# Optimization experiments

Measured on AMD Instinct MI355X. Metric: run time of the kernel, lower is better.

Reference implementation:

```python
import jax, jax.numpy as jnp
import numpy as np


def setup_inputs() -> dict:
    key = jax.random.key(0)
    k0, k1, k2, k3 = jax.random.split(key, 4)
    B, C, D, H, W = 2, 64, 48, 96, 96
    KS = 3
    x = jax.random.normal(k0, (B, C, D, H, W), jnp.float32)
    # Conv3d 1x1 kernels collapse to dense [out, in] matrices
    qkv_w = jax.random.normal(k1, (3 * C, C), jnp.float32) * (1.0 / np.sqrt(C))
    qkv_b = jnp.zeros((3 * C,), jnp.float32)
    out_w = jax.random.normal(k2, (C, C), jnp.float32) * (1.0 / np.sqrt(C))
    out_b = jnp.zeros((C,), jnp.float32)
    rel_pos = jax.random.normal(k3, (C, KS, KS, KS), jnp.float32)
    return {"x": x, "qkv_w": qkv_w, "qkv_b": qkv_b,
            "out_w": out_w, "out_b": out_b, "rel_pos": rel_pos}


def reference(x, qkv_w, qkv_b, out_w, out_b, rel_pos):
    B, C, D, H, W = x.shape
    ks = rel_pos.shape[1]
    p = ks // 2
    # 1x1x1 conv == per-voxel dense projection
    qkv = jnp.einsum('bcdhw,oc->bodhw', x, qkv_w) + qkv_b[None, :, None, None, None]
    Q, K, V = jnp.split(qkv, 3, axis=1)
    pad = ((0, 0), (0, 0), (p, p), (p, p), (p, p))
    Kp = jnp.pad(K, pad)
    Vp = jnp.pad(V, pad)
    scale = 1.0 / np.sqrt(C)
    # attention logits over the ks^3 shifted windows (static slices, fixed small loop)
    logits = []
    for i in range(ks):
        for j in range(ks):
            for k in range(ks):
                Ks = Kp[:, :, i:i + D, j:j + H, k:k + W] \
                    + rel_pos[:, i, j, k][None, :, None, None, None]
                logits.append(jnp.sum(Q * Ks, axis=1) * scale)  # [B,D,H,W]
    attn = jax.nn.softmax(jnp.stack(logits, axis=1), axis=1)  # [B,ks^3,D,H,W]
    # weighted sum of shifted V windows, accumulated onto residual x (forward_v1)
    out = x
    idx = 0
    for i in range(ks):
        for j in range(ks):
            for k in range(ks):
                out = out + attn[:, idx][:, None] * Vp[:, :, i:i + D, j:j + H, k:k + W]
                idx += 1
    return jnp.einsum('bcdhw,oc->bodhw', out, out_w) + out_b[None, :, None, None, None]
```

## Files before the change

kernel.cpp:

```cpp
#include <hip/hip_runtime.h>
#include <hip/hip_bf16.h>

#define Sd 442368
#define HWc 9216
#define Wc 96
#define Hc 96
#define Dc 48

typedef unsigned short u16;
typedef unsigned int u32;
typedef __attribute__((ext_vector_type(8))) short short8;
typedef __attribute__((ext_vector_type(4))) float f32x4;

static __device__ __forceinline__ u16 f2bf(float f){
    __hip_bfloat16 h = __float2bfloat16(f);
    return *reinterpret_cast<u16*>(&h);
}
static __device__ __forceinline__ u32 pk2(float a, float b){
    return ((u32)f2bf(b) << 16) | (u32)f2bf(a);
}
static __device__ __forceinline__ float bflo(u32 u){ return __uint_as_float(u << 16); }
static __device__ __forceinline__ float bfhi(u32 u){ return __uint_as_float(u & 0xffff0000u); }

static __device__ __forceinline__ short8 ldfrag_w(const float* p){
    float4 f0 = *reinterpret_cast<const float4*>(p);
    float4 f1 = *reinterpret_cast<const float4*>(p + 4);
    union { short8 s; u32 u[4]; } r;
    r.u[0] = pk2(f0.x, f0.y); r.u[1] = pk2(f0.z, f0.w);
    r.u[2] = pk2(f1.x, f1.y); r.u[3] = pk2(f1.z, f1.w);
    return r.s;
}

#define NBLK_A 3456
__global__ __launch_bounds__(256, 2) void kv_mfma(
    const float* __restrict__ x, const float* __restrict__ qkv_w,
    const float* __restrict__ qkv_b, u16* __restrict__ KV)
{
    int bid = blockIdx.x;
    bid = (bid & 7) * (NBLK_A / 8) + (bid >> 3);
    int batch = bid / (NBLK_A / 2);
    int s0 = (bid - batch * (NBLK_A / 2)) * 256;
    int t = threadIdx.x, lane = t & 63, wv = t >> 6;
    int lo = lane & 15, hi = lane >> 4;
    __shared__ u16 L[256 * 72];

    const float* xb = x + (size_t)batch * 64 * Sd + s0;
    {
        u32 pk[32];
#pragma unroll
        for (int c = 0; c < 64; c += 2){
            float f0 = xb[(size_t)c * Sd + t];
            float f1 = xb[(size_t)(c + 1) * Sd + t];
            pk[c >> 1] = pk2(f0, f1);
        }
#pragma unroll
        for (int k = 0; k < 8; ++k){
            uint4 u; u.x = pk[k*4+0]; u.y = pk[k*4+1]; u.z = pk[k*4+2]; u.w = pk[k*4+3];
            *reinterpret_cast<uint4*>(&L[t * 72 + k * 8]) = u;
        }
    }
    __syncthreads();

    short8 af[8][2];
    f32x4  bias[8];
#pragma unroll
    for (int mt = 0; mt < 8; ++mt){
#pragma unroll
        for (int kh = 0; kh < 2; ++kh)
            af[mt][kh] = ldfrag_w(qkv_w + (size_t)(64 + mt*16 + lo) * 64 + kh*32 + hi*8);
        bias[mt] = *reinterpret_cast<const f32x4*>(qkv_b + 64 + mt*16 + hi*4);
    }

#pragma unroll
    for (int nt = 0; nt < 4; ++nt){
        int vl = wv * 64 + nt * 16 + lo;
        const u16* br = &L[vl * 72 + hi * 8];
        short8 b0 = *reinterpret_cast<const short8*>(br);
        short8 b1 = *reinterpret_cast<const short8*>(br + 32);
        u16* kvrow = KV + (size_t)(batch * Sd + s0 + vl) * 128 + hi * 4;
#pragma unroll
        for (int mt = 0; mt < 8; ++mt){
            f32x4 acc = bias[mt];
            acc = __builtin_amdgcn_mfma_f32_16x16x32_bf16(af[mt][0], b0, acc, 0, 0, 0);
            acc = __builtin_amdgcn_mfma_f32_16x16x32_bf16(af[mt][1], b1, acc, 0, 0, 0);
            uint2 st; st.x = pk2(acc[0], acc[1]); st.y = pk2(acc[2], acc[3]);
            *reinterpret_cast<uint2*>(kvrow + mt * 16) = st;
        }
    }
}

#define NBLK_B 6912
__global__ __launch_bounds__(256, 4) void attn_mfma2(
    const float* __restrict__ x, const float* __restrict__ qkv_w,
    const float* __restrict__ qkv_b, const float* __restrict__ out_w,
    const float* __restrict__ out_b, const float* __restrict__ rel_pos,
    const u16* __restrict__ KV, float* __restrict__ out)
{
    int bid = blockIdx.x;
    bid = (bid & 7) * (NBLK_B / 8) + (bid >> 3);
    int batch = bid / (NBLK_B / 2);
    int s0 = (bid - batch * (NBLK_B / 2)) * 128;
    int t = threadIdx.x, lane = t & 63, wv = t >> 6;
    int lo = lane & 15, hi = lane >> 4;
    int vt = t >> 1, half = t & 1;

    __shared__ u16 Lx[128 * 72];
    __shared__ u16 Lq[128 * 72];
    float* Lr = reinterpret_cast<float*>(Lx);

    const float* xb = x + (size_t)batch * 64 * Sd + s0;
    {
        u32 pk[16];
#pragma unroll
        for (int c2 = 0; c2 < 32; c2 += 2){
            float f0 = xb[(size_t)(half*32 + c2) * Sd + vt];
            float f1 = xb[(size_t)(half*32 + c2 + 1) * Sd + vt];
            pk[c2 >> 1] = pk2(f0, f1);
        }
#pragma unroll
        for (int k = 0; k < 4; ++k){
            uint4 u; u.x = pk[k*4+0]; u.y = pk[k*4+1]; u.z = pk[k*4+2]; u.w = pk[k*4+3];
            *reinterpret_cast<uint4*>(&Lx[vt * 72 + half * 32 + k * 8]) = u;
        }
    }
    __syncthreads();

    {
        short8 qa[4][2];
        f32x4  qbias[4];
#pragma unroll
        for (int mt = 0; mt < 4; ++mt){
#pragma unroll
            for (int kh = 0; kh < 2; ++kh)
                qa[mt][kh] = ldfrag_w(qkv_w + (size_t)(mt*16 + lo) * 64 + kh*32 + hi*8);
            qbias[mt] = *reinterpret_cast<const f32x4*>(qkv_b + mt*16 + hi*4);
        }
#pragma unroll
        for (int nt = 0; nt < 2; ++nt){
            int vl = wv * 32 + nt * 16 + lo;
            const u16* br = &Lx[vl * 72 + hi * 8];
            short8 b0 = *reinterpret_cast<const short8*>(br);
            short8 b1 = *reinterpret_cast<const short8*>(br + 32);
#pragma unroll
            for (int mt = 0; mt < 4; ++mt){
                f32x4 acc = qbias[mt];
                acc = __builtin_amdgcn_mfma_f32_16x16x32_bf16(qa[mt][0], b0, acc, 0, 0, 0);
                acc = __builtin_amdgcn_mfma_f32_16x16x32_bf16(qa[mt][1], b1, acc, 0, 0, 0);
                uint2 st; st.x = pk2(acc[0], acc[1]); st.y = pk2(acc[2], acc[3]);
                *reinterpret_cast<uint2*>(&Lq[vl * 72 + mt * 16 + hi * 4]) = st;
            }
        }
    }
    __syncthreads();

    float acc[32], Q[32];
    {
        const u16* xr = &Lx[vt * 72 + half * 32];
        const u16* qr = &Lq[vt * 72 + half * 32];
#pragma unroll
        for (int k = 0; k < 4; ++k){
            uint4 xa = *reinterpret_cast<const uint4*>(xr + k * 8);
            uint4 qa = *reinterpret_cast<const uint4*>(qr + k * 8);
            acc[k*8+0] = bflo(xa.x); acc[k*8+1] = bfhi(xa.x);
            acc[k*8+2] = bflo(xa.y); acc[k*8+3] = bfhi(xa.y);
            acc[k*8+4] = bflo(xa.z); acc[k*8+5] = bfhi(xa.z);
            acc[k*8+6] = bflo(xa.w); acc[k*8+7] = bfhi(xa.w);
            Q[k*8+0] = bflo(qa.x); Q[k*8+1] = bfhi(qa.x);
            Q[k*8+2] = bflo(qa.y); Q[k*8+3] = bfhi(qa.y);
            Q[k*8+4] = bflo(qa.z); Q[k*8+5] = bfhi(qa.z);
            Q[k*8+6] = bflo(qa.w); Q[k*8+7] = bfhi(qa.w);
        }
    }
    __syncthreads();

    {
        short8 ra[2][2];
#pragma unroll
        for (int mt = 0; mt < 2; ++mt){
            int o = mt * 16 + lo;
#pragma unroll
            for (int kh = 0; kh < 2; ++kh){
                float f[8];
#pragma unroll
                for (int j = 0; j < 8; ++j){
                    int k = kh * 32 + hi * 8 + j;
                    f[j] = (o < 27) ? rel_pos[k * 27 + o] : 0.f;
                }
                union { short8 s; u32 u[4]; } r;
                r.u[0] = pk2(f[0], f[1]); r.u[1] = pk2(f[2], f[3]);
                r.u[2] = pk2(f[4], f[5]); r.u[3] = pk2(f[6], f[7]);
                ra[mt][kh] = r.s;
            }
        }
#pragma unroll
        for (int nt = 0; nt < 2; ++nt){
            int vl = wv * 32 + nt * 16 + lo;
            const u16* br = &Lq[vl * 72 + hi * 8];
            short8 b0 = *reinterpret_cast<const short8*>(br);
            short8 b1 = *reinterpret_cast<const short8*>(br + 32);
            f32x4 a0 = {0.f, 0.f, 0.f, 0.f};
            f32x4 a1 = {0.f, 0.f, 0.f, 0.f};
            a0 = __builtin_amdgcn_mfma_f32_16x16x32_bf16(ra[0][0], b0, a0, 0, 0, 0);
            a0 = __builtin_amdgcn_mfma_f32_16x16x32_bf16(ra[0][1], b1, a0, 0, 0, 0);
            a1 = __builtin_amdgcn_mfma_f32_16x16x32_bf16(ra[1][0], b0, a1, 0, 0, 0);
            a1 = __builtin_amdgcn_mfma_f32_16x16x32_bf16(ra[1][1], b1, a1, 0, 0, 0);
#pragma unroll
            for (int j = 0; j < 4; ++j)
                Lr[vl * 29 + hi * 4 + j] = a0[j];
#pragma unroll
            for (int j = 0; j < 4; ++j){
                int row = 16 + hi * 4 + j;
                if (row < 27) Lr[vl * 29 + row] = a1[j];
            }
        }
    }
    __syncthreads();

    int s = s0 + vt;
    int d = s / HWc; int r = s - d * HWc; int h = r / Wc; int w = r - h * Wc;
    const u16* kvb = KV + ((size_t)batch * Sd + s) * 128 + half * 32;

    float lg[27];
#pragma unroll
    for (int o = 0; o < 27; ++o){
        const int di = o / 9 - 1, dj = (o / 3) % 3 - 1, dk = o % 3 - 1;
        bool inb = ((unsigned)(d + di) < (unsigned)Dc) &&
                   ((unsigned)(h + dj) < (unsigned)Hc) &&
                   ((unsigned)(w + dk) < (unsigned)Wc);
        float dsum = 0.f;
        if (inb){
            const u16* kp = kvb + (ptrdiff_t)(di * HWc + dj * Wc + dk) * 128;
            float d0 = 0.f, d1 = 0.f, d2 = 0.f, d3 = 0.f;
#pragma unroll
            for (int k = 0; k < 4; ++k){
                uint4 kk = *reinterpret_cast<const uint4*>(kp + k * 8);
                d0 += bflo(kk.x) * Q[k*8+0]; d1 += bfhi(kk.x) * Q[k*8+1];
                d2 += bflo(kk.y) * Q[k*8+2]; d3 += bfhi(kk.y) * Q[k*8+3];
                d0 += bflo(kk.z) * Q[k*8+4]; d1 += bfhi(kk.z) * Q[k*8+5];
                d2 += bflo(kk.w) * Q[k*8+6]; d3 += bfhi(kk.w) * Q[k*8+7];
            }
            dsum = (d0 + d1) + (d2 + d3);
        }
        lg[o] = dsum;
    }
#pragma unroll
    for (int o = 0; o < 27; ++o){
        float other = __shfl_xor(lg[o], 1);
        lg[o] = 0.125f * (lg[o] + other + Lr[vt * 29 + o]);
    }

    float m = lg[0];
#pragma unroll
    for (int o = 1; o < 27; ++o) m = fmaxf(m, lg[o]);
    float ssum = 0.f;
#pragma unroll
    for (int o = 0; o < 27; ++o){ lg[o] = __expf(lg[o] - m); ssum += lg[o]; }
    float inv = 1.f / ssum;

#pragma unroll
    for (int o = 0; o < 27; ++o){
        const int di = o / 9 - 1, dj = (o / 3) % 3 - 1, dk = o % 3 - 1;
        bool inb = ((unsigned)(d + di) < (unsigned)Dc) &&
                   ((unsigned)(h + dj) < (unsigned)Hc) &&
                   ((unsigned)(w + dk) < (unsigned)Wc);
        if (!inb) continue;
        float a = lg[o] * inv;
        const u16* vp = kvb + (ptrdiff_t)(di * HWc + dj * Wc + dk) * 128 + 64;
#pragma unroll
        for (int k = 0; k < 4; ++k){
            uint4 vv = *reinterpret_cast<const uint4*>(vp + k * 8);
            acc[k*8+0] += a * bflo(vv.x); acc[k*8+1] += a * bfhi(vv.x);
            acc[k*8+2] += a * bflo(vv.y); acc[k*8+3] += a * bfhi(vv.y);
            acc[k*8+4] += a * bflo(vv.z); acc[k*8+5] += a * bfhi(vv.z);
            acc[k*8+6] += a * bflo(vv.w); acc[k*8+7] += a * bfhi(vv.w);
        }
    }

#pragma unroll
    for (int k = 0; k < 4; ++k){
        uint4 u;
        u.x = pk2(acc[k*8+0], acc[k*8+1]); u.y = pk2(acc[k*8+2], acc[k*8+3]);
        u.z = pk2(acc[k*8+4], acc[k*8+5]); u.w = pk2(acc[k*8+6], acc[k*8+7]);
        *reinterpret_cast<uint4*>(&Lq[vt * 72 + half * 32 + k * 8]) = u;
    }
    __syncthreads();

    {
        short8 oa[4][2];
        f32x4  obias[4];
#pragma unroll
        for (int mt = 0; mt < 4; ++mt){
#pragma unroll
            for (int kh = 0; kh < 2; ++kh)
                oa[mt][kh] = ldfrag_w(out_w + (size_t)(mt*16 + lo) * 64 + kh*32 + hi*8);
            obias[mt] = *reinterpret_cast<const f32x4*>(out_b + mt*16 + hi*4);
        }
#pragma unroll
        for (int nt = 0; nt < 2; ++nt){
            int vl = wv * 32 + nt * 16 + lo;
            const u16* br = &Lq[vl * 72 + hi * 8];
            short8 b0 = *reinterpret_cast<const short8*>(br);
            short8 b1 = *reinterpret_cast<const short8*>(br + 32);
#pragma unroll
            for (int mt = 0; mt < 4; ++mt){
                f32x4 a4 = obias[mt];
                a4 = __builtin_amdgcn_mfma_f32_16x16x32_bf16(oa[mt][0], b0, a4, 0, 0, 0);
                a4 = __builtin_amdgcn_mfma_f32_16x16x32_bf16(oa[mt][1], b1, a4, 0, 0, 0);
                float* op = out + ((size_t)batch * 64 + mt*16 + hi*4) * Sd + (s0 + vl);
                op[0]              = a4[0];
                op[(size_t)Sd]     = a4[1];
                op[(size_t)2*Sd]   = a4[2];
                op[(size_t)3*Sd]   = a4[3];
            }
        }
    }
}

extern "C" void kernel_launch(void* const* d_in, const int* in_sizes, int n_in,
                              void* d_out, int out_size, void* d_ws, size_t ws_size,
                              hipStream_t stream) {
    const float* x       = (const float*)d_in[0];
    const float* qkv_w   = (const float*)d_in[1];
    const float* qkv_b   = (const float*)d_in[2];
    const float* out_w   = (const float*)d_in[3];
    const float* out_b   = (const float*)d_in[4];
    const float* rel_pos = (const float*)d_in[5];
    float* out = (float*)d_out;
    u16* KV = (u16*)d_ws;

    kv_mfma<<<NBLK_A, 256, 0, stream>>>(x, qkv_w, qkv_b, KV);
    attn_mfma2<<<NBLK_B, 256, 0, stream>>>(x, qkv_w, qkv_b, out_w, out_b,
                                           rel_pos, KV, out);
}
```

Baseline: 690.0 us.

## Fuse logits, softmax and V accumulation into a single online-softmax pass

Replaces the two-pass neighbourhood loop (logits, then softmax, then weighted V) with one pass that loads K and V together per neighbour and keeps a lazily rescaled running max and sum. Neighbour addresses are clamped without branches, the math uses packed float2 operations, and the scale is folded into exp2. Block barriers are dropped where each wave only reads the shared-memory rows it wrote itself, and the residual is now read from global fp32. This cuts repeated K/V traffic and barrier stalls, but the lazy rescale adds wave-wide votes and extra registers.

Result: slower. 766.3 us (+11.1%).

```diff
diff --git a/kernel.cpp b/kernel.cpp
--- a/kernel.cpp
+++ b/kernel.cpp
@@ -11,6 +11,7 @@
 typedef unsigned int u32;
 typedef __attribute__((ext_vector_type(8))) short short8;
 typedef __attribute__((ext_vector_type(4))) float f32x4;
+typedef __attribute__((ext_vector_type(2))) float f32x2;
 
 static __device__ __forceinline__ u16 f2bf(float f){
     __hip_bfloat16 h = __float2bfloat16(f);
@@ -21,6 +22,9 @@
 }
 static __device__ __forceinline__ float bflo(u32 u){ return __uint_as_float(u << 16); }
 static __device__ __forceinline__ float bfhi(u32 u){ return __uint_as_float(u & 0xffff0000u); }
+static __device__ __forceinline__ f32x2 unp2(u32 u){
+    f32x2 r; r.x = __uint_as_float(u << 16); r.y = __uint_as_float(u & 0xffff0000u); return r;
+}
 
 static __device__ __forceinline__ short8 ldfrag_w(const float* p){
     float4 f0 = *reinterpret_cast<const float4*>(p);
@@ -59,7 +63,6 @@
             *reinterpret_cast<uint4*>(&L[t * 72 + k * 8]) = u;
         }
     }
-    __syncthreads();
 
     short8 af[8][2];
     f32x4  bias[8];
@@ -90,7 +93,9 @@
 }
 
 #define NBLK_B 6912
-__global__ __launch_bounds__(256, 4) void attn_mfma2(
+#define SCLOG 0.18033688011112042f
+
+__global__ __launch_bounds__(256, 4) void attn_fused(
     const float* __restrict__ x, const float* __restrict__ qkv_w,
     const float* __restrict__ qkv_b, const float* __restrict__ out_w,
     const float* __restrict__ out_b, const float* __restrict__ rel_pos,
@@ -104,9 +109,8 @@
     int lo = lane & 15, hi = lane >> 4;
     int vt = t >> 1, half = t & 1;
 
-    __shared__ u16 Lx[128 * 72];
-    __shared__ u16 Lq[128 * 72];
-    float* Lr = reinterpret_cast<float*>(Lx);
+    __shared__ u16  Lx[128 * 72];
+    __shared__ float Lr[128 * 27];
 
     const float* xb = x + (size_t)batch * 64 * Sd + s0;
     {
@@ -123,7 +127,6 @@
             *reinterpret_cast<uint4*>(&Lx[vt * 72 + half * 32 + k * 8]) = u;
         }
     }
-    __syncthreads();
 
     {
         short8 qa[4][2];
@@ -147,31 +150,10 @@
                 acc = __builtin_amdgcn_mfma_f32_16x16x32_bf16(qa[mt][0], b0, acc, 0, 0, 0);
                 acc = __builtin_amdgcn_mfma_f32_16x16x32_bf16(qa[mt][1], b1, acc, 0, 0, 0);
                 uint2 st; st.x = pk2(acc[0], acc[1]); st.y = pk2(acc[2], acc[3]);
-                *reinterpret_cast<uint2*>(&Lq[vl * 72 + mt * 16 + hi * 4]) = st;
+                *reinterpret_cast<uint2*>(&Lx[vl * 72 + mt * 16 + hi * 4]) = st;
             }
         }
     }
-    __syncthreads();
-
-    float acc[32], Q[32];
-    {
-        const u16* xr = &Lx[vt * 72 + half * 32];
-        const u16* qr = &Lq[vt * 72 + half * 32];
-#pragma unroll
-        for (int k = 0; k < 4; ++k){
-            uint4 xa = *reinterpret_cast<const uint4*>(xr + k * 8);
-            uint4 qa = *reinterpret_cast<const uint4*>(qr + k * 8);
-            acc[k*8+0] = bflo(xa.x); acc[k*8+1] = bfhi(xa.x);
-            acc[k*8+2] = bflo(xa.y); acc[k*8+3] = bfhi(xa.y);
-            acc[k*8+4] = bflo(xa.z); acc[k*8+5] = bfhi(xa.z);
-            acc[k*8+6] = bflo(xa.w); acc[k*8+7] = bfhi(xa.w);
-            Q[k*8+0] = bflo(qa.x); Q[k*8+1] = bfhi(qa.x);
-            Q[k*8+2] = bflo(qa.y); Q[k*8+3] = bfhi(qa.y);
-            Q[k*8+4] = bflo(qa.z); Q[k*8+5] = bfhi(qa.z);
-            Q[k*8+6] = bflo(qa.w); Q[k*8+7] = bfhi(qa.w);
-        }
-    }
-    __syncthreads();
 
     {
         short8 ra[2][2];
@@ -195,7 +177,7 @@
 #pragma unroll
         for (int nt = 0; nt < 2; ++nt){
             int vl = wv * 32 + nt * 16 + lo;
-            const u16* br = &Lq[vl * 72 + hi * 8];
+            const u16* br = &Lx[vl * 72 + hi * 8];
             short8 b0 = *reinterpret_cast<const short8*>(br);
             short8 b1 = *reinterpret_cast<const short8*>(br + 32);
             f32x4 a0 = {0.f, 0.f, 0.f, 0.f};
@@ -206,84 +188,120 @@
             a1 = __builtin_amdgcn_mfma_f32_16x16x32_bf16(ra[1][1], b1, a1, 0, 0, 0);
 #pragma unroll
             for (int j = 0; j < 4; ++j)
-                Lr[vl * 29 + hi * 4 + j] = a0[j];
+                Lr[vl * 27 + hi * 4 + j] = a0[j] * SCLOG;
 #pragma unroll
             for (int j = 0; j < 4; ++j){
                 int row = 16 + hi * 4 + j;
-                if (row < 27) Lr[vl * 29 + row] = a1[j];
+                if (row < 27) Lr[vl * 27 + row] = a1[j] * SCLOG;
             }
         }
     }
-    __syncthreads();
+
+    f32x2 q2[16];
+#pragma unroll
+    for (int k = 0; k < 4; ++k){
+        uint4 q4 = *reinterpret_cast<const uint4*>(&Lx[vt * 72 + half * 32 + k * 8]);
+        q2[k*4+0] = unp2(q4.x) * SCLOG;
+        q2[k*4+1] = unp2(q4.y) * SCLOG;
+        q2[k*4+2] = unp2(q4.z) * SCLOG;
+        q2[k*4+3] = unp2(q4.w) * SCLOG;
+    }
 
     int s = s0 + vt;
-    int d = s / HWc; int r = s - d * HWc; int h = r / Wc; int w = r - h * Wc;
-    const u16* kvb = KV + ((size_t)batch * Sd + s) * 128 + half * 32;
-
-    float lg[27];
+    int d = s / HWc; int r = s - d * HWc; int h3 = r / Wc; int w3 = r - h3 * Wc;
+
+    int cdm = (d  > 0)      ? -HWc : 0;
+    int cdp = (d  < Dc - 1) ?  HWc : 0;
+    int chm = (h3 > 0)      ? -Wc  : 0;
+    int chp = (h3 < Hc - 1) ?  Wc  : 0;
+    int cwm = (w3 > 0)      ? -1   : 0;
+    int cwp = (w3 < Wc - 1) ?  1   : 0;
+    bool vdm = d  > 0, vdp = d  < Dc - 1;
+    bool vhm = h3 > 0, vhp = h3 < Hc - 1;
+    bool vwm = w3 > 0, vwp = w3 < Wc - 1;
+
+    const char* KVc = reinterpret_cast<const char*>(KV);
+    int kbase = (batch * Sd + s) * 256 + half * 64;
+    const float* lr = &Lr[vt * 27];
+
+    float m = -1e30f, l = 0.f;
+    f32x2 acc[16];
+#pragma unroll
+    for (int i = 0; i < 16; ++i) acc[i] = (f32x2){0.f, 0.f};
+
 #pragma unroll
     for (int o = 0; o < 27; ++o){
         const int di = o / 9 - 1, dj = (o / 3) % 3 - 1, dk = o % 3 - 1;
-        bool inb = ((unsigned)(d + di) < (unsigned)Dc) &&
-                   ((unsigned)(h + dj) < (unsigned)Hc) &&
-                   ((unsigned)(w + dk) < (unsigned)Wc);
-        float dsum = 0.f;
-        if (inb){
-            const u16* kp = kvb + (ptrdiff_t)(di * HWc + dj * Wc + dk) * 128;
-            float d0 = 0.f, d1 = 0.f, d2 = 0.f, d3 = 0.f;
-#pragma unroll
-            for (int k = 0; k < 4; ++k){
-                uint4 kk = *reinterpret_cast<const uint4*>(kp + k * 8);
-                d0 += bflo(kk.x) * Q[k*8+0]; d1 += bfhi(kk.x) * Q[k*8+1];
-                d2 += bflo(kk.y) * Q[k*8+2]; d3 += bfhi(kk.y) * Q[k*8+3];
-                d0 += bflo(kk.z) * Q[k*8+4]; d1 += bfhi(kk.z) * Q[k*8+5];
-                d2 += bflo(kk.w) * Q[k*8+6]; d3 += bfhi(kk.w) * Q[k*8+7];
-            }
-            dsum = (d0 + d1) + (d2 + d3);
-        }
-        lg[o] = dsum;
-    }
-#pragma unroll
-    for (int o = 0; o < 27; ++o){
-        float other = __shfl_xor(lg[o], 1);
-        lg[o] = 0.125f * (lg[o] + other + Lr[vt * 29 + o]);
-    }
-
-    float m = lg[0];
-#pragma unroll
-    for (int o = 1; o < 27; ++o) m = fmaxf(m, lg[o]);
-    float ssum = 0.f;
-#pragma unroll
-    for (int o = 0; o < 27; ++o){ lg[o] = __expf(lg[o] - m); ssum += lg[o]; }
-    float inv = 1.f / ssum;
-
-#pragma unroll
-    for (int o = 0; o < 27; ++o){
-        const int di = o / 9 - 1, dj = (o / 3) % 3 - 1, dk = o % 3 - 1;
-        bool inb = ((unsigned)(d + di) < (unsigned)Dc) &&
-                   ((unsigned)(h + dj) < (unsigned)Hc) &&
-                   ((unsigned)(w + dk) < (unsigned)Wc);
-        if (!inb) continue;
-        float a = lg[o] * inv;
-        const u16* vp = kvb + (ptrdiff_t)(di * HWc + dj * Wc + dk) * 128 + 64;
+        int doff = (di < 0 ? cdm : di > 0 ? cdp : 0)
+                 + (dj < 0 ? chm : dj > 0 ? chp : 0)
+                 + (dk < 0 ? cwm : dk > 0 ? cwp : 0);
+        bool valid = (di < 0 ? vdm : di > 0 ? vdp : true)
+                  && (dj < 0 ? vhm : dj > 0 ? vhp : true)
+                  && (dk < 0 ? vwm : dk > 0 ? vwp : true);
+        const uint4* p4 = reinterpret_cast<const uint4*>(KVc + (kbase + doff * 256));
+
+        uint4 kk[4];
+#pragma unroll
+        for (int k = 0; k < 4; ++k) kk[k] = p4[k];
+        uint4 vv[4];
+#pragma unroll
+        for (int k = 0; k < 4; ++k) vv[k] = p4[8 + k];
+
+        f32x2 dd = {0.f, 0.f};
 #pragma unroll
         for (int k = 0; k < 4; ++k){
-            uint4 vv = *reinterpret_cast<const uint4*>(vp + k * 8);
-            acc[k*8+0] += a * bflo(vv.x); acc[k*8+1] += a * bfhi(vv.x);
-            acc[k*8+2] += a * bflo(vv.y); acc[k*8+3] += a * bfhi(vv.y);
-            acc[k*8+4] += a * bflo(vv.z); acc[k*8+5] += a * bfhi(vv.z);
-            acc[k*8+6] += a * bflo(vv.w); acc[k*8+7] += a * bfhi(vv.w);
-        }
-    }
-
-#pragma unroll
-    for (int k = 0; k < 4; ++k){
-        uint4 u;
-        u.x = pk2(acc[k*8+0], acc[k*8+1]); u.y = pk2(acc[k*8+2], acc[k*8+3]);
-        u.z = pk2(acc[k*8+4], acc[k*8+5]); u.w = pk2(acc[k*8+6], acc[k*8+7]);
-        *reinterpret_cast<uint4*>(&Lq[vt * 72 + half * 32 + k * 8]) = u;
-    }
-    __syncthreads();
+            dd += unp2(kk[k].x) * q2[k*4+0];
+            dd += unp2(kk[k].y) * q2[k*4+1];
+            dd += unp2(kk[k].z) * q2[k*4+2];
+            dd += unp2(kk[k].w) * q2[k*4+3];
+        }
+        float dot = dd.x + dd.y;
+        dot += __shfl_xor(dot, 1);
+        dot = valid ? dot : 0.f;
+        float lgm = dot + lr[o];
+
+        float mn = fmaxf(m, lgm);
+        if (__any(mn > m + 8.f)){
+            float sc = __builtin_amdgcn_exp2f(m - mn);
+            l *= sc;
+            f32x2 sc2 = {sc, sc};
+#pragma unroll
+            for (int i = 0; i < 16; ++i) acc[i] *= sc2;
+            m = mn;
+        }
+        float p = __builtin_amdgcn_exp2f(lgm - m);
+        l += p;
+        float pv = valid ? p : 0.f;
+        f32x2 p2 = {pv, pv};
+#pragma unroll
+        for (int k = 0; k < 4; ++k){
+            acc[k*4+0] += unp2(vv[k].x) * p2;
+            acc[k*4+1] += unp2(vv[k].y) * p2;
+            acc[k*4+2] += unp2(vv[k].z) * p2;
+            acc[k*4+3] += unp2(vv[k].w) * p2;
+        }
+    }
+
+    {
+        float inv = 1.f / l;
+        f32x2 inv2 = {inv, inv};
+        const float* xv = x + ((size_t)batch * 64 + half * 32) * Sd + (s0 + vt);
+#pragma unroll
+        for (int i = 0; i < 16; ++i){
+            acc[i] *= inv2;
+            acc[i].x += xv[(size_t)(2*i)     * Sd];
+            acc[i].y += xv[(size_t)(2*i + 1) * Sd];
+        }
+#pragma unroll
+        for (int k = 0; k < 4; ++k){
+            uint4 u;
+            u.x = pk2(acc[k*4+0].x, acc[k*4+0].y);
+            u.y = pk2(acc[k*4+1].x, acc[k*4+1].y);
+            u.z = pk2(acc[k*4+2].x, acc[k*4+2].y);
+            u.w = pk2(acc[k*4+3].x, acc[k*4+3].y);
+            *reinterpret_cast<uint4*>(&Lx[vt * 72 + half * 32 + k * 8]) = u;
+        }
+    }
 
     {
         short8 oa[4][2];
@@ -298,7 +316,7 @@
 #pragma unroll
         for (int nt = 0; nt < 2; ++nt){
             int vl = wv * 32 + nt * 16 + lo;
-            const u16* br = &Lq[vl * 72 + hi * 8];
+            const u16* br = &Lx[vl * 72 + hi * 8];
             short8 b0 = *reinterpret_cast<const short8*>(br);
             short8 b1 = *reinterpret_cast<const short8*>(br + 32);
 #pragma unroll
@@ -329,6 +347,6 @@
     u16* KV = (u16*)d_ws;
 
     kv_mfma<<<NBLK_A, 256, 0, stream>>>(x, qkv_w, qkv_b, KV);
-    attn_mfma2<<<NBLK_B, 256, 0, stream>>>(x, qkv_w, qkv_b, out_w, out_b,
+    attn_fused<<<NBLK_B, 256, 0, stream>>>(x, qkv_w, qkv_b, out_w, out_b,
                                            rel_pos, KV, out);
 }
```

## Split attention work four ways per voxel with wave-local tiles and fewer barriers

Applied to the files above, without the earlier changes.

The attention kernel now handles 64 voxels per block with four threads per voxel, each owning 16 channels, instead of 128 voxels with two threads per voxel. Q, K and V data are reduced with two shuffle steps, and relative-position logits are stored in bf16 LDS. Each wave now only touches LDS rows it wrote itself, so most block barriers are removed, including one in kv_mfma. LDS use drops and the occupancy hint rises to 6 blocks per CU, meant to hide the latency of KV gathers better. In exchange, the residual is re-read from fp32 global memory, and more shuffles and more blocks are needed.

After: 894.8 us. 1.3x slower.

```diff
diff --git a/kernel.cpp b/kernel.cpp
--- a/kernel.cpp
+++ b/kernel.cpp
@@ -59,7 +59,6 @@
             *reinterpret_cast<uint4*>(&L[t * 72 + k * 8]) = u;
         }
     }
-    __syncthreads();
 
     short8 af[8][2];
     f32x4  bias[8];
@@ -89,8 +88,8 @@
     }
 }
 
-#define NBLK_B 6912
-__global__ __launch_bounds__(256, 4) void attn_mfma2(
+#define NBLK_B 13824
+__global__ __launch_bounds__(256, 6) void attn4(
     const float* __restrict__ x, const float* __restrict__ qkv_w,
     const float* __restrict__ qkv_b, const float* __restrict__ out_w,
     const float* __restrict__ out_b, const float* __restrict__ rel_pos,
@@ -99,28 +98,29 @@
     int bid = blockIdx.x;
     bid = (bid & 7) * (NBLK_B / 8) + (bid >> 3);
     int batch = bid / (NBLK_B / 2);
-    int s0 = (bid - batch * (NBLK_B / 2)) * 128;
+    int s0 = (bid - batch * (NBLK_B / 2)) * 64;
     int t = threadIdx.x, lane = t & 63, wv = t >> 6;
     int lo = lane & 15, hi = lane >> 4;
-    int vt = t >> 1, half = t & 1;
-
-    __shared__ u16 Lx[128 * 72];
-    __shared__ u16 Lq[128 * 72];
-    float* Lr = reinterpret_cast<float*>(Lx);
+    int vt = t >> 2, q = t & 3;
+
+    __shared__ u16 Lx[64 * 72];
+    __shared__ u16 Lq[64 * 72];
+    __shared__ u16 Lr[64 * 28];
 
     const float* xb = x + (size_t)batch * 64 * Sd + s0;
     {
-        u32 pk[16];
-#pragma unroll
-        for (int c2 = 0; c2 < 32; c2 += 2){
-            float f0 = xb[(size_t)(half*32 + c2) * Sd + vt];
-            float f1 = xb[(size_t)(half*32 + c2 + 1) * Sd + vt];
+        int u = lane;
+        u32 pk[8];
+#pragma unroll
+        for (int c2 = 0; c2 < 16; c2 += 2){
+            float f0 = xb[(size_t)(wv*16 + c2) * Sd + u];
+            float f1 = xb[(size_t)(wv*16 + c2 + 1) * Sd + u];
             pk[c2 >> 1] = pk2(f0, f1);
         }
 #pragma unroll
-        for (int k = 0; k < 4; ++k){
-            uint4 u; u.x = pk[k*4+0]; u.y = pk[k*4+1]; u.z = pk[k*4+2]; u.w = pk[k*4+3];
-            *reinterpret_cast<uint4*>(&Lx[vt * 72 + half * 32 + k * 8]) = u;
+        for (int k2 = 0; k2 < 2; ++k2){
+            uint4 uu; uu.x = pk[k2*4+0]; uu.y = pk[k2*4+1]; uu.z = pk[k2*4+2]; uu.w = pk[k2*4+3];
+            *reinterpret_cast<uint4*>(&Lx[u * 72 + wv * 16 + k2 * 8]) = uu;
         }
     }
     __syncthreads();
@@ -135,43 +135,19 @@
                 qa[mt][kh] = ldfrag_w(qkv_w + (size_t)(mt*16 + lo) * 64 + kh*32 + hi*8);
             qbias[mt] = *reinterpret_cast<const f32x4*>(qkv_b + mt*16 + hi*4);
         }
-#pragma unroll
-        for (int nt = 0; nt < 2; ++nt){
-            int vl = wv * 32 + nt * 16 + lo;
-            const u16* br = &Lx[vl * 72 + hi * 8];
-            short8 b0 = *reinterpret_cast<const short8*>(br);
-            short8 b1 = *reinterpret_cast<const short8*>(br + 32);
-#pragma unroll
-            for (int mt = 0; mt < 4; ++mt){
-                f32x4 acc = qbias[mt];
-                acc = __builtin_amdgcn_mfma_f32_16x16x32_bf16(qa[mt][0], b0, acc, 0, 0, 0);
-                acc = __builtin_amdgcn_mfma_f32_16x16x32_bf16(qa[mt][1], b1, acc, 0, 0, 0);
-                uint2 st; st.x = pk2(acc[0], acc[1]); st.y = pk2(acc[2], acc[3]);
-                *reinterpret_cast<uint2*>(&Lq[vl * 72 + mt * 16 + hi * 4]) = st;
-            }
-        }
-    }
-    __syncthreads();
-
-    float acc[32], Q[32];
-    {
-        const u16* xr = &Lx[vt * 72 + half * 32];
-        const u16* qr = &Lq[vt * 72 + half * 32];
-#pragma unroll
-        for (int k = 0; k < 4; ++k){
-            uint4 xa = *reinterpret_cast<const uint4*>(xr + k * 8);
-            uint4 qa = *reinterpret_cast<const uint4*>(qr + k * 8);
-            acc[k*8+0] = bflo(xa.x); acc[k*8+1] = bfhi(xa.x);
-            acc[k*8+2] = bflo(xa.y); acc[k*8+3] = bfhi(xa.y);
-            acc[k*8+4] = bflo(xa.z); acc[k*8+5] = bfhi(xa.z);
-            acc[k*8+6] = bflo(xa.w); acc[k*8+7] = bfhi(xa.w);
-            Q[k*8+0] = bflo(qa.x); Q[k*8+1] = bfhi(qa.x);
-            Q[k*8+2] = bflo(qa.y); Q[k*8+3] = bfhi(qa.y);
-            Q[k*8+4] = bflo(qa.z); Q[k*8+5] = bfhi(qa.z);
-            Q[k*8+6] = bflo(qa.w); Q[k*8+7] = bfhi(qa.w);
-        }
-    }
-    __syncthreads();
+        int vl = wv * 16 + lo;
+        const u16* br = &Lx[vl * 72 + hi * 8];
+        short8 b0 = *reinterpret_cast<const short8*>(br);
+        short8 b1 = *reinterpret_cast<const short8*>(br + 32);
+#pragma unroll
+        for (int mt = 0; mt < 4; ++mt){
+            f32x4 acc = qbias[mt];
+            acc = __builtin_amdgcn_mfma_f32_16x16x32_bf16(qa[mt][0], b0, acc, 0, 0, 0);
+            acc = __builtin_amdgcn_mfma_f32_16x16x32_bf16(qa[mt][1], b1, acc, 0, 0, 0);
+            uint2 st; st.x = pk2(acc[0], acc[1]); st.y = pk2(acc[2], acc[3]);
+            *reinterpret_cast<uint2*>(&Lq[vl * 72 + mt * 16 + hi * 4]) = st;
+        }
+    }
 
     {
         short8 ra[2][2];
@@ -192,61 +168,71 @@
                 ra[mt][kh] = r.s;
             }
         }
-#pragma unroll
-        for (int nt = 0; nt < 2; ++nt){
-            int vl = wv * 32 + nt * 16 + lo;
-            const u16* br = &Lq[vl * 72 + hi * 8];
-            short8 b0 = *reinterpret_cast<const short8*>(br);
-            short8 b1 = *reinterpret_cast<const short8*>(br + 32);
-            f32x4 a0 = {0.f, 0.f, 0.f, 0.f};
-            f32x4 a1 = {0.f, 0.f, 0.f, 0.f};
-            a0 = __builtin_amdgcn_mfma_f32_16x16x32_bf16(ra[0][0], b0, a0, 0, 0, 0);
-            a0 = __builtin_amdgcn_mfma_f32_16x16x32_bf16(ra[0][1], b1, a0, 0, 0, 0);
-            a1 = __builtin_amdgcn_mfma_f32_16x16x32_bf16(ra[1][0], b0, a1, 0, 0, 0);
-            a1 = __builtin_amdgcn_mfma_f32_16x16x32_bf16(ra[1][1], b1, a1, 0, 0, 0);
-#pragma unroll
-            for (int j = 0; j < 4; ++j)
-                Lr[vl * 29 + hi * 4 + j] = a0[j];
-#pragma unroll
-            for (int j = 0; j < 4; ++j){
-                int row = 16 + hi * 4 + j;
-                if (row < 27) Lr[vl * 29 + row] = a1[j];
-            }
-        }
-    }
-    __syncthreads();
+        int vl = wv * 16 + lo;
+        const u16* br = &Lq[vl * 72 + hi * 8];
+        short8 b0 = *reinterpret_cast<const short8*>(br);
+        short8 b1 = *reinterpret_cast<const short8*>(br + 32);
+        f32x4 a0 = {0.f, 0.f, 0.f, 0.f};
+        f32x4 a1 = {0.f, 0.f, 0.f, 0.f};
+        a0 = __builtin_amdgcn_mfma_f32_16x16x32_bf16(ra[0][0], b0, a0, 0, 0, 0);
+        a0 = __builtin_amdgcn_mfma_f32_16x16x32_bf16(ra[0][1], b1, a0, 0, 0, 0);
+        a1 = __builtin_amdgcn_mfma_f32_16x16x32_bf16(ra[1][0], b0, a1, 0, 0, 0);
+        a1 = __builtin_amdgcn_mfma_f32_16x16x32_bf16(ra[1][1], b1, a1, 0, 0, 0);
+        u32* Lr32 = reinterpret_cast<u32*>(Lr);
+        Lr32[vl * 14 + hi * 2 + 0] = pk2(a0[0], a0[1]);
+        Lr32[vl * 14 + hi * 2 + 1] = pk2(a0[2], a0[3]);
+        if (hi < 3){
+            Lr32[vl * 14 + 8 + hi * 2 + 0] = pk2(a1[0], a1[1]);
+            Lr32[vl * 14 + 8 + hi * 2 + 1] = pk2(a1[2], a1[3]);
+        }
+    }
+
+    float Q[16];
+    {
+        const u16* qr = &Lq[vt * 72 + q * 16];
+        uint4 qa0 = *reinterpret_cast<const uint4*>(qr);
+        uint4 qa1 = *reinterpret_cast<const uint4*>(qr + 8);
+        Q[0]  = bflo(qa0.x); Q[1]  = bfhi(qa0.x);
+        Q[2]  = bflo(qa0.y); Q[3]  = bfhi(qa0.y);
+        Q[4]  = bflo(qa0.z); Q[5]  = bfhi(qa0.z);
+        Q[6]  = bflo(qa0.w); Q[7]  = bfhi(qa0.w);
+        Q[8]  = bflo(qa1.x); Q[9]  = bfhi(qa1.x);
+        Q[10] = bflo(qa1.y); Q[11] = bfhi(qa1.y);
+        Q[12] = bflo(qa1.z); Q[13] = bfhi(qa1.z);
+        Q[14] = bflo(qa1.w); Q[15] = bfhi(qa1.w);
+    }
 
     int s = s0 + vt;
-    int d = s / HWc; int r = s - d * HWc; int h = r / Wc; int w = r - h * Wc;
-    const u16* kvb = KV + ((size_t)batch * Sd + s) * 128 + half * 32;
+    int d = s / HWc; int r = s - d * HWc; int h3 = r / Wc; int w3 = r - h3 * Wc;
+    const u16* kvb = KV + ((size_t)batch * Sd + (size_t)s) * 128 + q * 16;
+    const u16* lr = &Lr[vt * 28];
 
     float lg[27];
 #pragma unroll
     for (int o = 0; o < 27; ++o){
         const int di = o / 9 - 1, dj = (o / 3) % 3 - 1, dk = o % 3 - 1;
         bool inb = ((unsigned)(d + di) < (unsigned)Dc) &&
-                   ((unsigned)(h + dj) < (unsigned)Hc) &&
-                   ((unsigned)(w + dk) < (unsigned)Wc);
+                   ((unsigned)(h3 + dj) < (unsigned)Hc) &&
+                   ((unsigned)(w3 + dk) < (unsigned)Wc);
         float dsum = 0.f;
         if (inb){
-            const u16* kp = kvb + (ptrdiff_t)(di * HWc + dj * Wc + dk) * 128;
+            const uint4* p4 = reinterpret_cast<const uint4*>(kvb + (ptrdiff_t)(di * HWc + dj * Wc + dk) * 128);
+            uint4 k0 = p4[0];
+            uint4 k1 = p4[1];
             float d0 = 0.f, d1 = 0.f, d2 = 0.f, d3 = 0.f;
-#pragma unroll
-            for (int k = 0; k < 4; ++k){
-                uint4 kk = *reinterpret_cast<const uint4*>(kp + k * 8);
-                d0 += bflo(kk.x) * Q[k*8+0]; d1 += bfhi(kk.x) * Q[k*8+1];
-                d2 += bflo(kk.y) * Q[k*8+2]; d3 += bfhi(kk.y) * Q[k*8+3];
-                d0 += bflo(kk.z) * Q[k*8+4]; d1 += bfhi(kk.z) * Q[k*8+5];
-                d2 += bflo(kk.w) * Q[k*8+6]; d3 += bfhi(kk.w) * Q[k*8+7];
-            }
+            d0 += bflo(k0.x) * Q[0];  d1 += bfhi(k0.x) * Q[1];
+            d2 += bflo(k0.y) * Q[2];  d3 += bfhi(k0.y) * Q[3];
+            d0 += bflo(k0.z) * Q[4];  d1 += bfhi(k0.z) * Q[5];
+            d2 += bflo(k0.w) * Q[6];  d3 += bfhi(k0.w) * Q[7];
+            d0 += bflo(k1.x) * Q[8];  d1 += bfhi(k1.x) * Q[9];
+            d2 += bflo(k1.y) * Q[10]; d3 += bfhi(k1.y) * Q[11];
+            d0 += bflo(k1.z) * Q[12]; d1 += bfhi(k1.z) * Q[13];
+            d2 += bflo(k1.w) * Q[14]; d3 += bfhi(k1.w) * Q[15];
             dsum = (d0 + d1) + (d2 + d3);
         }
-        lg[o] = dsum;
-    }
-#pragma unroll
-    for (int o = 0; o < 27; ++o){
-        float other = __shfl_xor(lg[o], 1);
-        lg[o] = 0.125f * (lg[o] + other + Lr[vt * 29 + o]);
+        dsum += __shfl_xor(dsum, 1);
+        dsum += __shfl_xor(dsum, 2);
+        lg[o] = 0.125f * (dsum + __uint_as_float(((u32)lr[o]) << 16));
     }
 
     float m = lg[0];
@@ -257,33 +243,45 @@
     for (int o = 0; o < 27; ++o){ lg[o] = __expf(lg[o] - m); ssum += lg[o]; }
     float inv = 1.f / ssum;
 
+    float acc[16];
+#pragma unroll
+    for (int c = 0; c < 16; ++c) acc[c] = 0.f;
 #pragma unroll
     for (int o = 0; o < 27; ++o){
         const int di = o / 9 - 1, dj = (o / 3) % 3 - 1, dk = o % 3 - 1;
         bool inb = ((unsigned)(d + di) < (unsigned)Dc) &&
-                   ((unsigned)(h + dj) < (unsigned)Hc) &&
-                   ((unsigned)(w + dk) < (unsigned)Wc);
+                   ((unsigned)(h3 + dj) < (unsigned)Hc) &&
+                   ((unsigned)(w3 + dk) < (unsigned)Wc);
         if (!inb) continue;
         float a = lg[o] * inv;
-        const u16* vp = kvb + (ptrdiff_t)(di * HWc + dj * Wc + dk) * 128 + 64;
-#pragma unroll
-        for (int k = 0; k < 4; ++k){
-            uint4 vv = *reinterpret_cast<const uint4*>(vp + k * 8);
-            acc[k*8+0] += a * bflo(vv.x); acc[k*8+1] += a * bfhi(vv.x);
-            acc[k*8+2] += a * bflo(vv.y); acc[k*8+3] += a * bfhi(vv.y);
-            acc[k*8+4] += a * bflo(vv.z); acc[k*8+5] += a * bfhi(vv.z);
-            acc[k*8+6] += a * bflo(vv.w); acc[k*8+7] += a * bfhi(vv.w);
-        }
-    }
-
-#pragma unroll
-    for (int k = 0; k < 4; ++k){
-        uint4 u;
-        u.x = pk2(acc[k*8+0], acc[k*8+1]); u.y = pk2(acc[k*8+2], acc[k*8+3]);
-        u.z = pk2(acc[k*8+4], acc[k*8+5]); u.w = pk2(acc[k*8+6], acc[k*8+7]);
-        *reinterpret_cast<uint4*>(&Lq[vt * 72 + half * 32 + k * 8]) = u;
-    }
-    __syncthreads();
+        const uint4* p4 = reinterpret_cast<const uint4*>(kvb + (ptrdiff_t)(di * HWc + dj * Wc + dk) * 128 + 64);
+        uint4 v0 = p4[0];
+        uint4 v1 = p4[1];
+        acc[0]  += a * bflo(v0.x); acc[1]  += a * bfhi(v0.x);
+        acc[2]  += a * bflo(v0.y); acc[3]  += a * bfhi(v0.y);
+        acc[4]  += a * bflo(v0.z); acc[5]  += a * bfhi(v0.z);
+        acc[6]  += a * bflo(v0.w); acc[7]  += a * bfhi(v0.w);
+        acc[8]  += a * bflo(v1.x); acc[9]  += a * bfhi(v1.x);
+        acc[10] += a * bflo(v1.y); acc[11] += a * bfhi(v1.y);
+        acc[12] += a * bflo(v1.z); acc[13] += a * bfhi(v1.z);
+        acc[14] += a * bflo(v1.w); acc[15] += a * bfhi(v1.w);
+    }
+
+    {
+        const float* xv = x + ((size_t)batch * 64 + q * 16) * Sd + (size_t)(s0 + vt);
+#pragma unroll
+        for (int c = 0; c < 16; ++c) acc[c] += xv[(size_t)c * Sd];
+    }
+
+    {
+        uint4 w0, w1;
+        w0.x = pk2(acc[0],  acc[1]);  w0.y = pk2(acc[2],  acc[3]);
+        w0.z = pk2(acc[4],  acc[5]);  w0.w = pk2(acc[6],  acc[7]);
+        w1.x = pk2(acc[8],  acc[9]);  w1.y = pk2(acc[10], acc[11]);
+        w1.z = pk2(acc[12], acc[13]); w1.w = pk2(acc[14], acc[15]);
+        *reinterpret_cast<uint4*>(&Lq[vt * 72 + q * 16])     = w0;
+        *reinterpret_cast<uint4*>(&Lq[vt * 72 + q * 16 + 8]) = w1;
+    }
 
     {
         short8 oa[4][2];
@@ -295,23 +293,20 @@
                 oa[mt][kh] = ldfrag_w(out_w + (size_t)(mt*16 + lo) * 64 + kh*32 + hi*8);
             obias[mt] = *reinterpret_cast<const f32x4*>(out_b + mt*16 + hi*4);
         }
-#pragma unroll
-        for (int nt = 0; nt < 2; ++nt){
-            int vl = wv * 32 + nt * 16 + lo;
-            const u16* br = &Lq[vl * 72 + hi * 8];
-            short8 b0 = *reinterpret_cast<const short8*>(br);
-            short8 b1 = *reinterpret_cast<const short8*>(br + 32);
-#pragma unroll
-            for (int mt = 0; mt < 4; ++mt){
-                f32x4 a4 = obias[mt];
-                a4 = __builtin_amdgcn_mfma_f32_16x16x32_bf16(oa[mt][0], b0, a4, 0, 0, 0);
-                a4 = __builtin_amdgcn_mfma_f32_16x16x32_bf16(oa[mt][1], b1, a4, 0, 0, 0);
-                float* op = out + ((size_t)batch * 64 + mt*16 + hi*4) * Sd + (s0 + vl);
-                op[0]              = a4[0];
-                op[(size_t)Sd]     = a4[1];
-                op[(size_t)2*Sd]   = a4[2];
-                op[(size_t)3*Sd]   = a4[3];
-            }
+        int vl = wv * 16 + lo;
+        const u16* br = &Lq[vl * 72 + hi * 8];
+        short8 b0 = *reinterpret_cast<const short8*>(br);
+        short8 b1 = *reinterpret_cast<const short8*>(br + 32);
+#pragma unroll
+        for (int mt = 0; mt < 4; ++mt){
+            f32x4 a4 = obias[mt];
+            a4 = __builtin_amdgcn_mfma_f32_16x16x32_bf16(oa[mt][0], b0, a4, 0, 0, 0);
+            a4 = __builtin_amdgcn_mfma_f32_16x16x32_bf16(oa[mt][1], b1, a4, 0, 0, 0);
+            float* op = out + ((size_t)batch * 64 + mt*16 + hi*4) * Sd + (s0 + vl);
+            op[0]              = a4[0];
+            op[(size_t)Sd]     = a4[1];
+            op[(size_t)2*Sd]   = a4[2];
+            op[(size_t)3*Sd]   = a4[3];
         }
     }
 }
@@ -329,6 +324,6 @@
     u16* KV = (u16*)d_ws;
 
     kv_mfma<<<NBLK_A, 256, 0, stream>>>(x, qkv_w, qkv_b, KV);
-    attn_mfma2<<<NBLK_B, 256, 0, stream>>>(x, qkv_w, qkv_b, out_w, out_b,
-                                           rel_pos, KV, out);
-}
+    attn4<<<NBLK_B, 256, 0, stream>>>(x, qkv_w, qkv_b, out_w, out_b,
+                                      rel_pos, KV, out);
+}
```
